# Kernel optimization log

Hardware: AMD Instinct MI355X
Metric: run time of the kernel (lower is better)

Reference implementation:

```python
import jax, jax.numpy as jnp
import numpy as np
import math

N_EMBD = 1024
N_HEAD = 16
HEAD_DIM = N_EMBD // N_HEAD

def setup_inputs() -> dict:
    key = jax.random.key(0)
    ks = jax.random.split(key, 9)
    B, T, C = 2, 2048, N_EMBD
    s = 1.0 / math.sqrt(C)
    return {
        "x": jax.random.normal(ks[0], (B, T, C), dtype=jnp.float32),
        "Wq": jax.random.normal(ks[1], (C, C), dtype=jnp.float32) * s,
        "bq": jnp.zeros((C,), dtype=jnp.float32),
        "Wk": jax.random.normal(ks[2], (C, C), dtype=jnp.float32) * s,
        "bk": jnp.zeros((C,), dtype=jnp.float32),
        "Wv": jax.random.normal(ks[3], (C, C), dtype=jnp.float32) * s,
        "bv": jnp.zeros((C,), dtype=jnp.float32),
        "Wp": jax.random.normal(ks[4], (C, C), dtype=jnp.float32) * s,
        "bp": jnp.zeros((C,), dtype=jnp.float32),
    }

def reference(x, Wq, bq, Wk, bk, Wv, bv, Wp, bp):
    B, T, C = x.shape
    H, D = N_HEAD, HEAD_DIM
    q = (x @ Wq + bq).reshape(B, T, H, D).transpose(0, 2, 1, 3)  # [B,H,T,D]
    k = (x @ Wk + bk).reshape(B, T, H, D).transpose(0, 2, 1, 3)
    v = (x @ Wv + bv).reshape(B, T, H, D).transpose(0, 2, 1, 3)
    att = jnp.einsum('bhqd,bhkd->bhqk', q, k) / math.sqrt(D)
    causal = jnp.tril(jnp.ones((T, T), dtype=bool))
    att = jnp.where(causal, att, -jnp.inf)
    att = jax.nn.softmax(att, axis=-1)
    att = jnp.nan_to_num(att)
    y = jnp.einsum('bhqk,bhkd->bhqd', att, v)
    y = y.transpose(0, 2, 1, 3).reshape(B, T, C)
    return y @ Wp + bp
```

## Files before the change

### kernel.cpp

```cpp
#include <hip/hip_runtime.h>
#include <hip/hip_bf16.h>
#include <stdint.h>

typedef unsigned short u16;
typedef __attribute__((ext_vector_type(8))) short short8;
typedef __attribute__((ext_vector_type(4))) float f32x4;

static __device__ __forceinline__ u16 f2bf(float f) {
  unsigned u = __builtin_bit_cast(unsigned, f);
  u += 0x7fffu + ((u >> 16) & 1u);
  return (u16)(u >> 16);
}

static __device__ __forceinline__ unsigned cvtpk(float lo, float hi) {
  unsigned r;
  asm("v_cvt_pk_bf16_f32 %0, %1, %2" : "=v"(r) : "v"(lo), "v"(hi));
  return r;
}

static __device__ __forceinline__ void gload16(const u16* g, u16* l) {
  __builtin_amdgcn_global_load_lds(
      (__attribute__((address_space(1))) void*)const_cast<u16*>(g),
      (__attribute__((address_space(3))) void*)l, 16, 0, 0);
}

__global__ __launch_bounds__(256) void prep_kernel(
    const float* __restrict__ x, const float* __restrict__ Wq,
    const float* __restrict__ Wk, const float* __restrict__ Wv,
    const float* __restrict__ Wp, u16* __restrict__ xb, u16* __restrict__ wt) {
  __shared__ float tile[64][65];
  int b = blockIdx.x;
  if (b < 2048) {
    size_t i = (size_t)b * 256 + threadIdx.x;
    const float4* xp = (const float4*)x + i * 2;
    float4 a = xp[0], v = xp[1];
    union { u16 u[8]; int4 q; } r;
    r.u[0] = f2bf(a.x); r.u[1] = f2bf(a.y); r.u[2] = f2bf(a.z); r.u[3] = f2bf(a.w);
    r.u[4] = f2bf(v.x); r.u[5] = f2bf(v.y); r.u[6] = f2bf(v.z); r.u[7] = f2bf(v.w);
    *(int4*)(xb + i * 8) = r.q;
  } else {
    int wb = b - 2048;
    int wz = wb >> 8, r8 = wb & 255;
    const float* W = (wz == 0) ? Wq : (wz == 1) ? Wk : (wz == 2) ? Wv : Wp;
    int n0 = (r8 & 15) * 64, k0 = (r8 >> 4) * 64;
    int tx = threadIdx.x & 63, ty = threadIdx.x >> 6;
#pragma unroll
    for (int r = 0; r < 16; ++r)
      tile[ty + 4 * r][tx] = W[(size_t)(k0 + ty + 4 * r) * 1024 + n0 + tx];
    __syncthreads();
    u16* dst = wt + (size_t)wz * 1024 * 1024;
#pragma unroll
    for (int r = 0; r < 16; ++r) {
      int n = ty + 4 * r;
      dst[(size_t)(n0 + n) * 1024 + k0 + tx] = f2bf(tile[tx][n]);
    }
  }
}

__global__ __launch_bounds__(256, 2) void gemm_qkv_kernel(
    const u16* __restrict__ A, const u16* __restrict__ Bt, int Kdim,
    int GM, int GN, int RM, int RN,
    u16* __restrict__ qd, u16* __restrict__ kd, u16* __restrict__ vd,
    const float* __restrict__ bq, const float* __restrict__ bk,
    const float* __restrict__ bv) {
  __shared__ u16 Alds[8192];
  __shared__ u16 Blds[8192];
  int tid = threadIdx.x;
  int lane = tid & 63, w = tid >> 6;
  int l15 = lane & 15, lg = lane >> 4;
  int flat = blockIdx.x;
  int xcd = flat & 7, idx = flat >> 3;
  int rnc = GN / RN;
  int rm = (xcd / rnc) * RM, rn = (xcd % rnc) * RN;
  int im = idx % RM, in_ = idx / RM;
  int m0 = (rm + im) * 128, n0 = (rn + in_) * 128;
  int wm = (w >> 1) * 64, wn = (w & 1) * 64;
  int srow = lane >> 3;
  int colsw = ((lane & 7) * 8) ^ ((srow & 7) * 8);

  const u16* pA[4];
  const u16* pB[4];
  int dls[4];
#pragma unroll
  for (int j = 0; j < 4; ++j) {
    int issue = w * 4 + j;
    int row = issue * 8 + srow;
    pA[j] = A + (size_t)(m0 + row) * Kdim + colsw;
    pB[j] = Bt + (size_t)(n0 + row) * Kdim + colsw;
    dls[j] = issue * 512;
  }
  int kx = (l15 & 7) << 4;
  int ofs0 = (lg * 16) ^ kx, ofs1 = (64 + lg * 16) ^ kx;
  int rbA = (wm + l15) * 128, rbB = (wn + l15) * 128;

  f32x4 acc[4][4] = {};
  for (int kt = 0; kt < Kdim; kt += 64) {
#pragma unroll
    for (int j = 0; j < 4; ++j) {
      gload16(pA[j], Alds + dls[j]);
      gload16(pB[j], Blds + dls[j]);
      pA[j] += 64; pB[j] += 64;
    }
    __syncthreads();
    __builtin_amdgcn_s_setprio(1);
#pragma unroll
    for (int kk = 0; kk < 2; ++kk) {
      int o_ = kk ? ofs1 : ofs0;
      short8 a[4], b[4];
#pragma unroll
      for (int mt = 0; mt < 4; ++mt)
        a[mt] = *(const short8*)((const char*)Alds + (rbA + o_) + mt * 2048);
#pragma unroll
      for (int nt = 0; nt < 4; ++nt)
        b[nt] = *(const short8*)((const char*)Blds + (rbB + o_) + nt * 2048);
#pragma unroll
      for (int mt = 0; mt < 4; ++mt)
#pragma unroll
        for (int nt = 0; nt < 4; ++nt)
          acc[mt][nt] = __builtin_amdgcn_mfma_f32_16x16x32_bf16(a[mt], b[nt],
                                                                acc[mt][nt], 0, 0, 0);
    }
    __builtin_amdgcn_s_setprio(0);
    __syncthreads();
  }
#pragma unroll
  for (int nt = 0; nt < 4; ++nt) {
    int n = n0 + wn + nt * 16 + l15;
    int wi = n >> 10, nn = n & 1023, h = nn >> 6, d = nn & 63;
    const float* bb = (wi == 0) ? bq : (wi == 1) ? bk : bv;
    float bval = bb[nn];
    if (wi == 2) {
#pragma unroll
      for (int mt = 0; mt < 4; ++mt) {
        int m = m0 + wm + mt * 16 + lg * 4;
        int mb = m >> 11, t = m & 2047;
        unsigned lo = cvtpk(acc[mt][nt][0] + bval, acc[mt][nt][1] + bval);
        unsigned hi = cvtpk(acc[mt][nt][2] + bval, acc[mt][nt][3] + bval);
        *(uint2*)&vd[((size_t)(mb * 16 + h) * 64 + d) * 2048 + t] =
            make_uint2(lo, hi);
      }
    } else {
      u16* dst = (wi == 0) ? qd : kd;
#pragma unroll
      for (int mt = 0; mt < 4; ++mt) {
#pragma unroll
        for (int i = 0; i < 4; ++i) {
          int m = m0 + wm + mt * 16 + lg * 4 + i;
          int mb = m >> 11, t = m & 2047;
          dst[((size_t)(mb * 16 + h) * 2048 + t) * 64 + d] =
              f2bf(acc[mt][nt][i] + bval);
        }
      }
    }
  }
}

__global__ __launch_bounds__(256, 2) void gemm_proj_kernel(
    const u16* __restrict__ A, const u16* __restrict__ Bt,
    float* __restrict__ outf, const float* __restrict__ bias1) {
  __shared__ u16 Alds[2 * 8192];
  __shared__ u16 Blds[2 * 4096];
  int tid = threadIdx.x;
  int lane = tid & 63, w = tid >> 6;
  int l15 = lane & 15, lg = lane >> 4;
  int flat = blockIdx.x;
  int xcd = flat & 7, idx = flat >> 3;
  int rm = (xcd >> 1) * 8, rn = (xcd & 1) * 8;
  int m0 = (rm + (idx & 7)) * 128, n0 = (rn + (idx >> 3)) * 64;
  int wm = (w >> 1) * 64, wn = (w & 1) * 32;
  int srow = lane >> 3;
  int colsw = ((lane & 7) * 8) ^ ((srow & 7) * 8);

  const u16* pA[4];
  int dlsA[4];
#pragma unroll
  for (int j = 0; j < 4; ++j) {
    int issue = w * 4 + j;
    int row = issue * 8 + srow;
    pA[j] = A + (size_t)(m0 + row) * 1024 + colsw;
    dlsA[j] = issue * 512;
  }
  const u16* pB[2];
  int dlsB[2];
#pragma unroll
  for (int it = 0; it < 2; ++it) {
    int chunk = it * 256 + tid;
    int row = chunk >> 3;
    int col = ((chunk & 7) * 8) ^ ((row & 7) * 8);
    pB[it] = Bt + (size_t)(n0 + row) * 1024 + col;
    dlsB[it] = (it * 256 + w * 64) * 8;
  }
  int kx = (l15 & 7) << 4;
  int ofs0 = (lg * 16) ^ kx, ofs1 = (64 + lg * 16) ^ kx;
  int rbA = (wm + l15) * 128, rbB = (wn + l15) * 128;

  auto stage = [&](int buf) {
    u16* Ad = Alds + buf * 8192;
    u16* Bd = Blds + buf * 4096;
#pragma unroll
    for (int j = 0; j < 4; ++j) { gload16(pA[j], Ad + dlsA[j]); pA[j] += 64; }
#pragma unroll
    for (int it = 0; it < 2; ++it) { gload16(pB[it], Bd + dlsB[it]); pB[it] += 64; }
  };

  f32x4 acc[4][2] = {};
  stage(0);
  int cur = 0;
  for (int kt = 0; kt < 1024; kt += 64) {
    __syncthreads();
    if (kt + 64 < 1024) stage(cur ^ 1);
    const char* Al = (const char*)Alds + cur * 16384;
    const char* Bl = (const char*)Blds + cur * 8192;
    __builtin_amdgcn_s_setprio(1);
#pragma unroll
    for (int kk = 0; kk < 2; ++kk) {
      int o_ = kk ? ofs1 : ofs0;
      short8 a[4], b[2];
#pragma unroll
      for (int mt = 0; mt < 4; ++mt)
        a[mt] = *(const short8*)(Al + (rbA + o_) + mt * 2048);
#pragma unroll
      for (int nt = 0; nt < 2; ++nt)
        b[nt] = *(const short8*)(Bl + (rbB + o_) + nt * 2048);
#pragma unroll
      for (int mt = 0; mt < 4; ++mt)
#pragma unroll
        for (int nt = 0; nt < 2; ++nt)
          acc[mt][nt] = __builtin_amdgcn_mfma_f32_16x16x32_bf16(a[mt], b[nt],
                                                                acc[mt][nt], 0, 0, 0);
    }
    __builtin_amdgcn_s_setprio(0);
    cur ^= 1;
  }
#pragma unroll
  for (int nt = 0; nt < 2; ++nt) {
    int n = n0 + wn + nt * 16 + l15;
    float bval = bias1[n];
#pragma unroll
    for (int mt = 0; mt < 4; ++mt) {
#pragma unroll
      for (int i = 0; i < 4; ++i) {
        int m = m0 + wm + mt * 16 + lg * 4 + i;
        outf[(size_t)m * 1024 + n] = acc[mt][nt][i] + bval;
      }
    }
  }
}

__global__ __launch_bounds__(256, 4) void fattn_kernel(const u16* __restrict__ qb,
                                                       const u16* __restrict__ kb,
                                                       const u16* __restrict__ vt,
                                                       u16* __restrict__ y) {
  __shared__ u16 Klds[2 * 4096];
  __shared__ u16 Vlds[2 * 4096];
  __shared__ u16 Plds[4 * 1024];
  int tid = threadIdx.x, lane = tid & 63, w = tid >> 6;
  int l15 = lane & 15, lg = lane >> 4;
  int flat = blockIdx.x;
  int bh = flat & 31;
  int qt = 31 - (flat >> 5);
  size_t base = (size_t)bh * 2048 * 64;
  int mb = bh >> 4, h = bh & 15;
  const float SC = 0.125f * 1.44269504088896340736f;
  const float NINF = -__builtin_inff();

  int r0 = tid >> 3, c0 = ((tid & 7) * 8) ^ ((r0 & 7) << 3);
  int r1 = (256 + tid) >> 3, c1 = ((tid & 7) * 8) ^ ((r1 & 7) << 3);
  const u16* pK0 = kb + base + (size_t)r0 * 64 + c0;
  const u16* pK1 = kb + base + (size_t)r1 * 64 + c1;
  const u16* pV0 = vt + base + (size_t)r0 * 2048 + c0;
  const u16* pV1 = vt + base + (size_t)r1 * 2048 + c1;
  int dk0 = w * 512, dk1 = (256 + w * 64) * 8;
  int kx = (l15 & 7) << 4;
  int rb0 = l15 * 128 + ((lg * 16) ^ kx);
  int rb1 = l15 * 128 + ((64 + lg * 16) ^ kx);
  char* pbase = (char*)Plds + w * 2048;
  int pw0 = l15 * 128 + ((lg * 8) ^ kx);
  int pw1 = l15 * 128 + ((32 + lg * 8) ^ kx);
  int pw2 = l15 * 128 + ((64 + lg * 8) ^ kx);
  int pw3 = l15 * 128 + ((96 + lg * 8) ^ kx);

  int qw = qt * 64 + w * 16;
  int qr = qw + l15;
  short8 qf[2];
#pragma unroll
  for (int kk = 0; kk < 2; ++kk)
    qf[kk] = *(const short8*)&qb[base + (size_t)qr * 64 + kk * 32 + lg * 8];
  f32x4 o[4] = {};
  float mrow = NINF, lrow = 0.f;
  {
    gload16(pK0, Klds + dk0); gload16(pK1, Klds + dk1);
    gload16(pV0, Vlds + dk0); gload16(pV1, Vlds + dk1);
    pK0 += 4096; pK1 += 4096; pV0 += 64; pV1 += 64;
  }
  int cb = 0;
  int ntiles = qt + 1;
  for (int j = 0; j < ntiles; ++j) {
    __syncthreads();
    if (j + 1 < ntiles) {
      u16* kd_ = Klds + (cb ^ 1) * 4096;
      u16* vd_ = Vlds + (cb ^ 1) * 4096;
      gload16(pK0, kd_ + dk0); gload16(pK1, kd_ + dk1);
      gload16(pV0, vd_ + dk0); gload16(pV1, vd_ + dk1);
      pK0 += 4096; pK1 += 4096; pV0 += 64; pV1 += 64;
    }
    const char* kl = (const char*)Klds + cb * 8192;
    const char* vl = (const char*)Vlds + cb * 8192;
    f32x4 s[4] = {};
    __builtin_amdgcn_s_setprio(1);
#pragma unroll
    for (int kk = 0; kk < 2; ++kk) {
      int o_ = kk ? rb1 : rb0;
      short8 ka[4];
#pragma unroll
      for (int nt = 0; nt < 4; ++nt)
        ka[nt] = *(const short8*)(kl + o_ + nt * 2048);
#pragma unroll
      for (int nt = 0; nt < 4; ++nt)
        s[nt] = __builtin_amdgcn_mfma_f32_16x16x32_bf16(ka[nt], qf[kk], s[nt], 0, 0, 0);
    }
    __builtin_amdgcn_s_setprio(0);
    float rs[16];
    if (j == qt) {
      int k0 = j * 64;
#pragma unroll
      for (int nt = 0; nt < 4; ++nt)
#pragma unroll
        for (int i = 0; i < 4; ++i) {
          int ka_ = k0 + nt * 16 + lg * 4 + i;
          rs[nt * 4 + i] = (ka_ > qr) ? NINF : s[nt][i];
        }
    } else {
#pragma unroll
      for (int nt = 0; nt < 4; ++nt)
#pragma unroll
        for (int i = 0; i < 4; ++i) rs[nt * 4 + i] = s[nt][i];
    }
    float rmax = fmaxf(
        fmaxf(fmaxf(fmaxf(rs[0], rs[1]), fmaxf(rs[2], rs[3])),
              fmaxf(fmaxf(rs[4], rs[5]), fmaxf(rs[6], rs[7]))),
        fmaxf(fmaxf(fmaxf(rs[8], rs[9]), fmaxf(rs[10], rs[11])),
              fmaxf(fmaxf(rs[12], rs[13]), fmaxf(rs[14], rs[15]))));
    float tmax = rmax * SC;
    if (!__all(tmax <= mrow + 8.f)) {
      float t2 = fmaxf(tmax, __shfl_xor(tmax, 16));
      t2 = fmaxf(t2, __shfl_xor(t2, 32));
      float vmax = fmaxf(t2, mrow);
      float scale = exp2f(mrow - vmax);
      mrow = vmax;
      lrow *= scale;
#pragma unroll
      for (int dn = 0; dn < 4; ++dn) o[dn] *= scale;
    }
    float p[16];
#pragma unroll
    for (int u = 0; u < 16; ++u) p[u] = exp2f(fmaf(rs[u], SC, -mrow));
    float pr0 = ((p[0] + p[1]) + (p[2] + p[3])) + ((p[4] + p[5]) + (p[6] + p[7]));
    float pr1 = ((p[8] + p[9]) + (p[10] + p[11])) + ((p[12] + p[13]) + (p[14] + p[15]));
    lrow += pr0 + pr1;
    *(uint2*)(pbase + pw0) = make_uint2(cvtpk(p[0], p[1]), cvtpk(p[2], p[3]));
    *(uint2*)(pbase + pw1) = make_uint2(cvtpk(p[4], p[5]), cvtpk(p[6], p[7]));
    *(uint2*)(pbase + pw2) = make_uint2(cvtpk(p[8], p[9]), cvtpk(p[10], p[11]));
    *(uint2*)(pbase + pw3) = make_uint2(cvtpk(p[12], p[13]), cvtpk(p[14], p[15]));
    __builtin_amdgcn_s_setprio(1);
#pragma unroll
    for (int kk = 0; kk < 2; ++kk) {
      int o_ = kk ? rb1 : rb0;
      short8 ap = *(const short8*)(pbase + o_);
#pragma unroll
      for (int dn = 0; dn < 4; ++dn) {
        short8 bv_ = *(const short8*)(vl + o_ + dn * 2048);
        o[dn] = __builtin_amdgcn_mfma_f32_16x16x32_bf16(bv_, ap, o[dn], 0, 0, 0);
      }
    }
    __builtin_amdgcn_s_setprio(0);
    cb ^= 1;
  }
  lrow += __shfl_xor(lrow, 16);
  lrow += __shfl_xor(lrow, 32);
  float inv = 1.f / lrow;
  size_t rb = ((size_t)(mb * 2048 + qr)) * 1024 + (size_t)h * 64;
#pragma unroll
  for (int dn = 0; dn < 4; ++dn) {
    unsigned lo = cvtpk(o[dn][0] * inv, o[dn][1] * inv);
    unsigned hi = cvtpk(o[dn][2] * inv, o[dn][3] * inv);
    *(uint2*)&y[rb + dn * 16 + lg * 4] = make_uint2(lo, hi);
  }
}

extern "C" void kernel_launch(void* const* d_in, const int* in_sizes, int n_in,
                              void* d_out, int out_size, void* d_ws, size_t ws_size,
                              hipStream_t stream) {
  const float* x  = (const float*)d_in[0];
  const float* Wq = (const float*)d_in[1];
  const float* bq = (const float*)d_in[2];
  const float* Wk = (const float*)d_in[3];
  const float* bk = (const float*)d_in[4];
  const float* Wv = (const float*)d_in[5];
  const float* bv = (const float*)d_in[6];
  const float* Wp = (const float*)d_in[7];
  const float* bp = (const float*)d_in[8];
  float* out = (float*)d_out;
  char* ws = (char*)d_ws;
  u16* xb   = (u16*)(ws);
  u16* wt   = (u16*)(ws + ((size_t)8 << 20));
  u16* qbuf = (u16*)(ws + ((size_t)16 << 20));
  u16* kbuf = (u16*)(ws + ((size_t)24 << 20));
  u16* vtb  = (u16*)(ws + ((size_t)32 << 20));
  u16* ybuf = (u16*)(ws + ((size_t)40 << 20));

  prep_kernel<<<dim3(3072), dim3(256), 0, stream>>>(x, Wq, Wk, Wv, Wp, xb, wt);
  gemm_qkv_kernel<<<dim3(768), dim3(256), 0, stream>>>(
      xb, wt, 1024, 32, 24, 8, 12, qbuf, kbuf, vtb, bq, bk, bv);
  fattn_kernel<<<dim3(1024), dim3(256), 0, stream>>>(qbuf, kbuf, vtb, ybuf);
  gemm_proj_kernel<<<dim3(512), dim3(256), 0, stream>>>(
      ybuf, wt + (size_t)3 * 1024 * 1024, out, bp);
  (void)in_sizes; (void)n_in; (void)out_size; (void)ws_size;
}
```

Before: 102.4 us.

## Single-buffer K/V tiles in attention and interleave causal tile order across blocks

Replaces the double-buffered K/V LDS staging with single buffers, shrinking shared memory per block so more blocks can be resident per CU. The loads of the next tile are no longer overlapped with compute; each iteration loads, syncs, computes, and syncs again. It also remaps block index to query tile in a zigzag pattern so that heavy and light causal tiles are interleaved in launch order for better load balance. The added barrier and loss of prefetch overlap may raise latency per iteration.

```diff
diff --git a/kernel.cpp b/kernel.cpp
--- a/kernel.cpp
+++ b/kernel.cpp
@@ -251,14 +251,21 @@
                                                        const u16* __restrict__ kb,
                                                        const u16* __restrict__ vt,
                                                        u16* __restrict__ y) {
-  __shared__ u16 Klds[2 * 4096];
-  __shared__ u16 Vlds[2 * 4096];
-  __shared__ u16 Plds[4 * 1024];
+  __shared__ u16 Klds[4096];
+  __shared__ u16 Vlds[4096];
+  __shared__ u16 Plds[4096];
   int tid = threadIdx.x, lane = tid & 63, w = tid >> 6;
   int l15 = lane & 15, lg = lane >> 4;
   int flat = blockIdx.x;
   int bh = flat & 31;
-  int qt = 31 - (flat >> 5);
+  int g = flat >> 5;
+  int qt;
+  switch (g >> 3) {
+    case 0:  qt = 31 - g; break;
+    case 1:  qt = g - 8;  break;
+    case 2:  qt = 39 - g; break;
+    default: qt = g - 16; break;
+  }
   size_t base = (size_t)bh * 2048 * 64;
   int mb = bh >> 4, h = bh & 15;
   const float SC = 0.125f * 1.44269504088896340736f;
@@ -288,24 +295,12 @@
     qf[kk] = *(const short8*)&qb[base + (size_t)qr * 64 + kk * 32 + lg * 8];
   f32x4 o[4] = {};
   float mrow = NINF, lrow = 0.f;
-  {
+  int ntiles = qt + 1;
+  for (int j = 0; j < ntiles; ++j) {
     gload16(pK0, Klds + dk0); gload16(pK1, Klds + dk1);
     gload16(pV0, Vlds + dk0); gload16(pV1, Vlds + dk1);
     pK0 += 4096; pK1 += 4096; pV0 += 64; pV1 += 64;
-  }
-  int cb = 0;
-  int ntiles = qt + 1;
-  for (int j = 0; j < ntiles; ++j) {
-    __syncthreads();
-    if (j + 1 < ntiles) {
-      u16* kd_ = Klds + (cb ^ 1) * 4096;
-      u16* vd_ = Vlds + (cb ^ 1) * 4096;
-      gload16(pK0, kd_ + dk0); gload16(pK1, kd_ + dk1);
-      gload16(pV0, vd_ + dk0); gload16(pV1, vd_ + dk1);
-      pK0 += 4096; pK1 += 4096; pV0 += 64; pV1 += 64;
-    }
-    const char* kl = (const char*)Klds + cb * 8192;
-    const char* vl = (const char*)Vlds + cb * 8192;
+    __syncthreads();
     f32x4 s[4] = {};
     __builtin_amdgcn_s_setprio(1);
 #pragma unroll
@@ -314,7 +309,7 @@
       short8 ka[4];
 #pragma unroll
       for (int nt = 0; nt < 4; ++nt)
-        ka[nt] = *(const short8*)(kl + o_ + nt * 2048);
+        ka[nt] = *(const short8*)((const char*)Klds + o_ + nt * 2048);
 #pragma unroll
       for (int nt = 0; nt < 4; ++nt)
         s[nt] = __builtin_amdgcn_mfma_f32_16x16x32_bf16(ka[nt], qf[kk], s[nt], 0, 0, 0);
@@ -369,12 +364,12 @@
       short8 ap = *(const short8*)(pbase + o_);
 #pragma unroll
       for (int dn = 0; dn < 4; ++dn) {
-        short8 bv_ = *(const short8*)(vl + o_ + dn * 2048);
+        short8 bv_ = *(const short8*)((const char*)Vlds + o_ + dn * 2048);
         o[dn] = __builtin_amdgcn_mfma_f32_16x16x32_bf16(bv_, ap, o[dn], 0, 0, 0);
       }
     }
     __builtin_amdgcn_s_setprio(0);
-    cb ^= 1;
+    __syncthreads();
   }
   lrow += __shfl_xor(lrow, 16);
   lrow += __shfl_xor(lrow, 32);
```

Measured after the change: 101.5 us. No clear change (-0.8%).
